# Kernel tuning notes

Hardware: AMD Instinct MI355X
Metric: run time of the kernel (lower is better)

## Reference

```python
import jax, jax.numpy as jnp
import numpy as np

HIDDEN = 1024
NUM_HEADS = 16
HEAD_DIM = HIDDEN // NUM_HEADS
EPS = 1e-12


def _layernorm(x, g, b):
    mu = jnp.mean(x, axis=-1, keepdims=True)
    var = jnp.var(x, axis=-1, keepdims=True)
    return (x - mu) * jax.lax.rsqrt(var + EPS) * g + b


def _attention(q, k, v, mask, Wd, bd, ln_g, ln_b):
    # q: [B,T,H], k/v: [B,S,H], mask: [B,1,1,S] additive
    B, T, _ = q.shape
    S = k.shape[1]
    qh = q.reshape(B, T, NUM_HEADS, HEAD_DIM).transpose(0, 2, 1, 3)  # [B,h,T,d]
    kh = k.reshape(B, S, NUM_HEADS, HEAD_DIM).transpose(0, 2, 1, 3)
    vh = v.reshape(B, S, NUM_HEADS, HEAD_DIM).transpose(0, 2, 1, 3)
    scores = jnp.einsum('bhtd,bhsd->bhts', qh, kh) / jnp.sqrt(jnp.float32(HEAD_DIM))
    if mask is not None:
        scores = scores + mask
    probs = jax.nn.softmax(scores, axis=-1)  # dropout = identity in eval
    ctx = jnp.einsum('bhts,bhsd->bthd', probs, vh)  # [B,T,h,d]
    # torch: w = dense.weight.t().view(h, d, H); einsum('bfnd,ndh->bfh')
    w = Wd.T.reshape(NUM_HEADS, HEAD_DIM, HIDDEN)
    proj = jnp.einsum('bthd,hdH->btH', ctx, w) + bd
    # residual is the (projected) query tensor q, per source
    return _layernorm(q + proj, ln_g, ln_b)


def setup_inputs() -> dict:
    key = jax.random.key(0)
    ks = jax.random.split(key, 12)
    s = 0.02
    B, S, T = 4, 1024, 1024
    return {
        'encoder_states': jax.random.normal(ks[0], (B, S, HIDDEN), jnp.float32),
        'decoder_inputs': jax.random.normal(ks[1], (B, T, HIDDEN), jnp.float32),
        'src_attention_mask': jnp.zeros((B, 1, 1, S), jnp.float32),
        'tgt_attention_mask': jnp.zeros((B, 1, 1, T), jnp.float32),
        'Wq': jax.random.normal(ks[2], (HIDDEN, HIDDEN), jnp.float32) * s,
        'bq': jnp.zeros((HIDDEN,), jnp.float32),
        'Wk': jax.random.normal(ks[3], (HIDDEN, HIDDEN), jnp.float32) * s,
        'bk': jnp.zeros((HIDDEN,), jnp.float32),
        'Wv': jax.random.normal(ks[4], (HIDDEN, HIDDEN), jnp.float32) * s,
        'bv': jnp.zeros((HIDDEN,), jnp.float32),
        'Wd': jax.random.normal(ks[5], (HIDDEN, HIDDEN), jnp.float32) * s,
        'bd': jnp.zeros((HIDDEN,), jnp.float32),
        'ln_g': jnp.ones((HIDDEN,), jnp.float32),
        'ln_b': jnp.zeros((HIDDEN,), jnp.float32),
    }


def reference(encoder_states, decoder_inputs, src_attention_mask, tgt_attention_mask,
              Wq, bq, Wk, bk, Wv, bv, Wd, bd, ln_g, ln_b):
    # projections (torch Linear: x @ W.T + b)
    q1 = decoder_inputs @ Wq.T + bq
    k1 = decoder_inputs @ Wk.T + bk
    v1 = decoder_inputs @ Wv.T + bv
    ek = encoder_states @ Wk.T + bk
    ev = encoder_states @ Wv.T + bv
    # self-attention over decoder states
    self_out = _attention(q1, k1, v1, tgt_attention_mask, Wd, bd, ln_g, ln_b)
    # cross-attention: query = self_out directly (no extra projection, per source)
    out = _attention(self_out, ek, ev, src_attention_mask, Wd, bd, ln_g, ln_b)
    return out
```

## Files before the change

kernel.cpp:

```cpp
#include <hip/hip_runtime.h>
#include <stdint.h>


#define B_   4
#define T_   1024
#define S_   1024
#define H_   1024
#define LOG2E 1.44269504088896340736f
#define SCALE_K (0.125f * LOG2E)

typedef __attribute__((ext_vector_type(8)))  __bf16       bf16x8;
typedef __attribute__((ext_vector_type(4)))  float        f32x4;
typedef __attribute__((ext_vector_type(16))) float        f32x16;
typedef __attribute__((ext_vector_type(4)))  unsigned int uint4v;

static __device__ __forceinline__ float bf2f(unsigned int u) {
    return __builtin_bit_cast(float, u << 16);
}
static __device__ __forceinline__ unsigned short f2bf(float f) {
    unsigned int x = __builtin_bit_cast(unsigned int, f);
    return (unsigned short)((x + 0x7fffu + ((x >> 16) & 1u)) >> 16);
}
static __device__ __forceinline__ unsigned int cvt_pk_bf16(float lo, float hi) {
    unsigned int r;
    asm("v_cvt_pk_bf16_f32 %0, %1, %2" : "=v"(r) : "v"(lo), "v"(hi));
    return r;
}
static __device__ __forceinline__ void perm32swap(unsigned int& a, unsigned int& b) {
    asm("v_permlane32_swap_b32 %0, %1" : "+v"(a), "+v"(b));
}
static __device__ __forceinline__ f32x4 mfma16(bf16x8 a, bf16x8 b, f32x4 c) {
    return __builtin_amdgcn_mfma_f32_16x16x32_bf16(a, b, c, 0, 0, 0);
}
static __device__ __forceinline__ f32x16 mfma32(bf16x8 a, bf16x8 b, f32x16 c) {
    return __builtin_amdgcn_mfma_f32_32x32x16_bf16(a, b, c, 0, 0, 0);
}

typedef const __attribute__((address_space(1))) void gv_t;
typedef __attribute__((address_space(3))) void lv_t;
static __device__ __forceinline__ void g2lds16(const void* g, void* l) {
    __builtin_amdgcn_global_load_lds((gv_t*)(size_t)g, (lv_t*)(unsigned int)(size_t)l, 16, 0, 0);
}

struct CvtArgs {
    const float* src[6];
    unsigned short* dst[6];
    float scale[6];
    int n4[6];
};
__global__ __launch_bounds__(256)
void cvt_multi(CvtArgs a) {
    const int k = blockIdx.y;
    const int i = blockIdx.x * 256 + threadIdx.x;
    if (i >= a.n4[k]) return;
    const float s = a.scale[k];
    float4 v = ((const float4*)a.src[k])[i];
    uint2 o;
    o.x = (unsigned)f2bf(v.x * s) | ((unsigned)f2bf(v.y * s) << 16);
    o.y = (unsigned)f2bf(v.z * s) | ((unsigned)f2bf(v.w * s) << 16);
    ((uint2*)a.dst[k])[i] = o;
}

struct GemmJob {
    const unsigned short* A[5];
    const unsigned short* W[5];
    const float* bias[5];
    float bs[5];
    unsigned short* O[5];
    unsigned short* OT[5];
};
__global__ __launch_bounds__(256, 2)
void gemm_bf16(GemmJob job)
{
    __shared__ char smem[32768];
    char* As = smem;
    char* Bs = smem + 16384;
    const int tid = threadIdx.x;
    const int lane = tid & 63;
    const int w = tid >> 6;
    const int c = lane & 15, g = lane >> 4;
    const int wm = (w >> 1) * 64, wn = (w & 1) * 64;
    const int m0 = blockIdx.x * 128;
    const int set = blockIdx.y >> 3;
    const int n0 = (blockIdx.y & 7) * 128;
    const unsigned short* A    = job.A[set];
    const unsigned short* W    = job.W[set];
    const float* bias          = job.bias[set];
    const float bscale         = job.bs[set];
    unsigned short* O          = job.O[set];
    unsigned short* OT         = job.OT[set];

    f32x4 acc[4][4];
#pragma unroll
    for (int i = 0; i < 4; i++)
#pragma unroll
        for (int j = 0; j < 4; j++) acc[i][j] = (f32x4){0.f, 0.f, 0.f, 0.f};

    const int srow = w * 32 + (lane >> 3);
    const int swzc = ((lane & 7) ^ (lane >> 3)) * 8;
    const unsigned short* gA = A + (size_t)(m0 + srow) * 1024 + swzc;
    const unsigned short* gB = W + (size_t)(n0 + srow) * 1024 + swzc;
    char* lA = As + w * 4096;
    char* lB = Bs + w * 4096;

    for (int kk = 0; kk < 1024; kk += 64) {
#pragma unroll
        for (int q = 0; q < 4; q++) {
            g2lds16(gA + kk + q*8192, lA + q*1024);
            g2lds16(gB + kk + q*8192, lB + q*1024);
        }
        __syncthreads();
#pragma unroll
        for (int ksub = 0; ksub < 2; ksub++) {
            bf16x8 af[4], bfr[4];
#pragma unroll
            for (int t = 0; t < 4; t++) {
                const int ra = wm + t*16 + c;
                const int rb = wn + t*16 + c;
                const int so = ((ksub*4 + g) ^ (c & 7)) << 4;
                af[t]  = *(const bf16x8*)(As + ra*128 + so);
                bfr[t] = *(const bf16x8*)(Bs + rb*128 + so);
            }
#pragma unroll
            for (int i = 0; i < 4; i++)
#pragma unroll
                for (int j = 0; j < 4; j++)
                    acc[i][j] = mfma16(af[i], bfr[j], acc[i][j]);
        }
        __syncthreads();
    }

    float bvv[4];
#pragma unroll
    for (int j = 0; j < 4; j++) bvv[j] = bias[n0 + wn + j*16 + c] * bscale;
    char* eb = As + w * 4096;
#pragma unroll
    for (int p = 0; p < 2; p++) {
#pragma unroll
        for (int ii = 0; ii < 2; ii++) {
            const int i = p*2 + ii;
#pragma unroll
            for (int j = 0; j < 4; j++)
#pragma unroll
                for (int r = 0; r < 4; r++)
                    *(unsigned short*)(eb + (ii*16 + g*4 + r)*128 + (c + j*16)*2)
                        = f2bf(acc[i][j][r] + bvv[j]);
        }
        asm volatile("s_waitcnt lgkmcnt(0)" ::: "memory");
        if (OT == nullptr) {
#pragma unroll
            for (int it = 0; it < 4; it++) {
                const int lrow = it*8 + (lane >> 3);
                uint4 vv = *(const uint4*)(eb + lrow*128 + (lane & 7)*16);
                *(uint4*)(O + (size_t)(m0 + wm + p*32 + lrow)*1024 + n0 + wn + (lane & 7)*8) = vv;
            }
        } else {
            const int n_glob = n0 + wn + lane;
            const int hh = n_glob >> 6, dd = n_glob & 63;
            const int bidx = m0 >> 10;
            const int s_base = (m0 & 1023) + wm + p*32;
            unsigned short* vout = OT + ((size_t)((bidx*16 + hh)*64 + dd))*S_ + s_base;
            unsigned int pk[16];
#pragma unroll
            for (int r = 0; r < 16; r++) {
                unsigned int lo = *(const unsigned short*)(eb + (2*r    )*128 + lane*2);
                unsigned int hi = *(const unsigned short*)(eb + (2*r + 1)*128 + lane*2);
                pk[r] = lo | (hi << 16);
            }
#pragma unroll
            for (int q = 0; q < 4; q++) {
                uint4 vv;
                vv.x = pk[q*4 + 0]; vv.y = pk[q*4 + 1];
                vv.z = pk[q*4 + 2]; vv.w = pk[q*4 + 3];
                *(uint4*)(vout + q*8) = vv;
            }
        }
        if (p == 0) asm volatile("s_waitcnt lgkmcnt(0)" ::: "memory");
    }
}

__global__ __launch_bounds__(256, 4)
void attn_fused2(const unsigned short* __restrict__ Q,
                 const unsigned short* __restrict__ Kx,
                 const unsigned short* __restrict__ VT,
                 const float* __restrict__ mask,
                 unsigned short* __restrict__ Octx)
{
    __shared__ char smem[32768 + 4096 + 512 + 16];
    float* mb   = (float*)(smem + 32768);
    float* lbuf = (float*)(smem + 32768 + 4096);
    int* flag   = (int*)(smem + 32768 + 4096 + 512);

    const int tid = threadIdx.x;
    const int lane = tid & 63, w = tid >> 6;
    const int qc = lane & 31, hi = lane >> 5;
    const int bh = blockIdx.y, b = bh >> 4, h = bh & 15;
    const int q0 = blockIdx.x * 128 + w * 32;

    const int r0 = tid >> 3, sg = tid & 7;
    const unsigned short* gK0 = Kx + (size_t)(b*S_ + r0)*H_  + h*64 + sg*8;
    const unsigned short* gK1 = gK0 + (size_t)32*H_;
    const unsigned short* gV0 = VT + (size_t)(bh*64 + r0)*S_ + sg*8;
    const unsigned short* gV1 = gV0 + (size_t)32*S_;
    const int woff = r0*128 + ((sg*16) ^ ((r0 & 7) << 4));

    const unsigned short* qptr = Q + (size_t)(b*T_ + q0 + qc)*H_ + h*64 + hi*8;
    bf16x8 qf[4];
#pragma unroll
    for (int s = 0; s < 4; s++) qf[s] = *(const bf16x8*)(qptr + s*16);

    uint4 cK0 = *(const uint4*)gK0;
    uint4 cK1 = *(const uint4*)gK1;
    uint4 cV0 = *(const uint4*)gV0;
    uint4 cV1 = *(const uint4*)gV1;

    if (tid == 0) *flag = 0;
    __syncthreads();
    {
        float4 mv = ((const float4*)(mask + (size_t)b*S_))[tid];
        float4 ms;
        ms.x = mv.x * LOG2E; ms.y = mv.y * LOG2E; ms.z = mv.z * LOG2E; ms.w = mv.w * LOG2E;
        ((float4*)mb)[tid] = ms;
        if (mv.x != 0.f || mv.y != 0.f || mv.z != 0.f || mv.w != 0.f) atomicOr(flag, 1);
    }
    {
        char* b0 = smem;
        *(uint4*)(b0 + woff)               = cK0;
        *(uint4*)(b0 + 4096 + woff)        = cK1;
        *(uint4*)(b0 + 8192 + woff)        = cV0;
        *(uint4*)(b0 + 8192 + 4096 + woff) = cV1;
    }
    __syncthreads();
    const int msk = *flag;

    f32x16 o0 = {}, o1 = {};
    float lacc = 0.f;

    for (int t = 0; t < 16; ++t) {
        uint4 nK0, nK1, nV0, nV1;
        if (t < 15) {
            const size_t ko = (size_t)(t + 1) * 64 * H_;
            const int    vo = (t + 1) * 64;
            nK0 = *(const uint4*)(gK0 + ko);
            nK1 = *(const uint4*)(gK1 + ko);
            nV0 = *(const uint4*)(gV0 + vo);
            nV1 = *(const uint4*)(gV1 + vo);
        }
        char* Ks = smem + (t & 1) * 16384;
        char* Vs = Ks + 8192;

#pragma unroll
        for (int ts = 0; ts < 2; ++ts) {
            f32x16 st = {};
            __builtin_amdgcn_s_setprio(1);
#pragma unroll
            for (int step = 0; step < 4; ++step) {
                bf16x8 ak = *(const bf16x8*)(Ks + (ts*32 + qc)*128 +
                             ((step*32 + hi*16) ^ ((qc & 7) << 4)));
                st = mfma32(ak, qf[step], st);
            }
            __builtin_amdgcn_s_setprio(0);

            float pv[16];
            if (msk) {
#pragma unroll
                for (int rq = 0; rq < 4; ++rq) {
                    const float4 bb = *(const float4*)(mb + t*64 + ts*32 + rq*8 + hi*4);
#pragma unroll
                    for (int e = 0; e < 4; ++e)
                        pv[rq*4 + e] = __builtin_amdgcn_exp2f(st[rq*4 + e] + (&bb.x)[e]);
                }
            } else {
#pragma unroll
                for (int r = 0; r < 16; ++r) pv[r] = __builtin_amdgcn_exp2f(st[r]);
            }
#pragma unroll
            for (int r = 0; r < 16; ++r) lacc += pv[r];

#pragma unroll
            for (int half = 0; half < 2; ++half) {
                unsigned w0 = cvt_pk_bf16(pv[half*8 + 0], pv[half*8 + 1]);
                unsigned w1 = cvt_pk_bf16(pv[half*8 + 2], pv[half*8 + 3]);
                unsigned w2 = cvt_pk_bf16(pv[half*8 + 4], pv[half*8 + 5]);
                unsigned w3 = cvt_pk_bf16(pv[half*8 + 6], pv[half*8 + 7]);
                perm32swap(w0, w2);
                perm32swap(w1, w3);
                uint4v fw; fw[0] = w0; fw[1] = w1; fw[2] = w2; fw[3] = w3;
                const bf16x8 pa = __builtin_bit_cast(bf16x8, fw);
                const int scol = (ts*64 + half*32 + hi*16) ^ ((qc & 7) << 4);
                bf16x8 v0 = *(const bf16x8*)(Vs + qc*128        + scol);
                bf16x8 v1 = *(const bf16x8*)(Vs + (32 + qc)*128 + scol);
                __builtin_amdgcn_s_setprio(1);
                o0 = mfma32(pa, v0, o0);
                o1 = mfma32(pa, v1, o1);
                __builtin_amdgcn_s_setprio(0);
            }
        }

        if (t < 15) {
            char* nxt = smem + ((t + 1) & 1) * 16384;
            *(uint4*)(nxt + woff)               = nK0;
            *(uint4*)(nxt + 4096 + woff)        = nK1;
            *(uint4*)(nxt + 8192 + woff)        = nV0;
            *(uint4*)(nxt + 8192 + 4096 + woff) = nV1;
        }
        __syncthreads();
    }

    {
        unsigned la = __builtin_bit_cast(unsigned, lacc);
        unsigned lb = la;
        perm32swap(la, lb);
        const float ltot = __builtin_bit_cast(float, la) + __builtin_bit_cast(float, lb);
        const float linv = 1.f / ltot;
        if (hi == 0) lbuf[w*32 + qc] = linv;
    }
    __syncthreads();
    float4 li[4];
#pragma unroll
    for (int rq = 0; rq < 4; ++rq)
        li[rq] = *(const float4*)(lbuf + w*32 + rq*8 + hi*4);

#pragma unroll
    for (int dt = 0; dt < 2; ++dt) {
        const f32x16& oo = dt ? o1 : o0;
#pragma unroll
        for (int r = 0; r < 16; ++r) {
            const int qrow = (r & 3) + 8*(r >> 2) + 4*hi;
            const float val = oo[r] * (&li[r >> 2].x)[r & 3];
            Octx[(size_t)(b*T_ + q0 + qrow)*H_ + h*64 + dt*32 + qc] = f2bf(val);
        }
    }
}

template<int OUTMODE>
__global__ __launch_bounds__(256)
void ln_kernel(const unsigned short* __restrict__ resid,
               const unsigned short* __restrict__ proj,
               const float* __restrict__ gam,
               const float* __restrict__ bet,
               unsigned short* __restrict__ obf,
               float* __restrict__ of32)
{
    __shared__ float red[8];
    const int tid = threadIdx.x;
    const int lane = tid & 63, w = tid >> 6;
    const int i = tid * 4;
    const size_t base = (size_t)blockIdx.x * 1024 + i;
    uint2 rv = *(const uint2*)(resid + base);
    uint2 pv = *(const uint2*)(proj + base);
    float x[4];
    x[0] = bf2f(rv.x & 0xffffu) + bf2f(pv.x & 0xffffu);
    x[1] = bf2f(rv.x >> 16)     + bf2f(pv.x >> 16);
    x[2] = bf2f(rv.y & 0xffffu) + bf2f(pv.y & 0xffffu);
    x[3] = bf2f(rv.y >> 16)     + bf2f(pv.y >> 16);
    float s = x[0] + x[1] + x[2] + x[3];
    float q = x[0]*x[0] + x[1]*x[1] + x[2]*x[2] + x[3]*x[3];
#pragma unroll
    for (int off = 1; off < 64; off <<= 1) {
        s += __shfl_xor(s, off);
        q += __shfl_xor(q, off);
    }
    if (lane == 0) { red[w*2] = s; red[w*2 + 1] = q; }
    __syncthreads();
    s = red[0] + red[2] + red[4] + red[6];
    q = red[1] + red[3] + red[5] + red[7];
    const float mu   = s * (1.f/1024.f);
    const float var  = q * (1.f/1024.f) - mu*mu;
    const float rstd = rsqrtf(var + 1e-12f);
    const float4 gv = *(const float4*)(gam + i);
    const float4 bv = *(const float4*)(bet + i);
    float y[4];
#pragma unroll
    for (int j = 0; j < 4; j++)
        y[j] = (x[j] - mu) * rstd * (&gv.x)[j] + (&bv.x)[j];
    if (OUTMODE == 0) {
        uint2 oo;
        oo.x = (unsigned)f2bf(y[0]) | ((unsigned)f2bf(y[1]) << 16);
        oo.y = (unsigned)f2bf(y[2]) | ((unsigned)f2bf(y[3]) << 16);
        *(uint2*)(obf + base) = oo;
    } else {
        float4 oo; oo.x = y[0]; oo.y = y[1]; oo.z = y[2]; oo.w = y[3];
        *(float4*)(of32 + base) = oo;
    }
}

extern "C" void kernel_launch(void* const* d_in, const int* in_sizes, int n_in,
                              void* d_out, int out_size, void* d_ws, size_t ws_size,
                              hipStream_t stream)
{
    const float* enc   = (const float*)d_in[0];
    const float* dec   = (const float*)d_in[1];
    const float* smask = (const float*)d_in[2];
    const float* tmask = (const float*)d_in[3];
    const float* Wq = (const float*)d_in[4];
    const float* bq = (const float*)d_in[5];
    const float* Wk = (const float*)d_in[6];
    const float* bk = (const float*)d_in[7];
    const float* Wv = (const float*)d_in[8];
    const float* bv = (const float*)d_in[9];
    const float* Wd = (const float*)d_in[10];
    const float* bd = (const float*)d_in[11];
    const float* lng = (const float*)d_in[12];
    const float* lnb = (const float*)d_in[13];
    float* out = (float*)d_out;

    char* ws = (char*)d_ws;
    const size_t MB = 1024ull * 1024ull;
    unsigned short* dec_bf = (unsigned short*)(ws + 0*MB);
    unsigned short* enc_bf = (unsigned short*)(ws + 8*MB);
    unsigned short* Wq_bf  = (unsigned short*)(ws + 16*MB);
    unsigned short* Wk_bf  = (unsigned short*)(ws + 18*MB);
    unsigned short* Wv_bf  = (unsigned short*)(ws + 20*MB);
    unsigned short* Wd_bf  = (unsigned short*)(ws + 22*MB);
    unsigned short* q1  = (unsigned short*)(ws + 24*MB);
    unsigned short* k1  = (unsigned short*)(ws + 32*MB);
    unsigned short* vt1 = (unsigned short*)(ws + 40*MB);
    unsigned short* ek  = (unsigned short*)(ws + 48*MB);
    unsigned short* evt = (unsigned short*)(ws + 56*MB);
    unsigned short* ctx      = dec_bf;
    unsigned short* proj     = enc_bf;
    unsigned short* self_out = k1;

    CvtArgs ca;
    ca.src[0] = dec; ca.dst[0] = dec_bf; ca.scale[0] = 1.f;      ca.n4[0] = 1048576;
    ca.src[1] = enc; ca.dst[1] = enc_bf; ca.scale[1] = 1.f;      ca.n4[1] = 1048576;
    ca.src[2] = Wq;  ca.dst[2] = Wq_bf;  ca.scale[2] = 1.f;      ca.n4[2] = 262144;
    ca.src[3] = Wk;  ca.dst[3] = Wk_bf;  ca.scale[3] = SCALE_K;  ca.n4[3] = 262144;
    ca.src[4] = Wv;  ca.dst[4] = Wv_bf;  ca.scale[4] = 1.f;      ca.n4[4] = 262144;
    ca.src[5] = Wd;  ca.dst[5] = Wd_bf;  ca.scale[5] = 1.f;      ca.n4[5] = 262144;
    cvt_multi<<<dim3(4096, 6), 256, 0, stream>>>(ca);

    GemmJob j1;
    j1.A[0] = dec_bf; j1.W[0] = Wq_bf; j1.bias[0] = bq; j1.bs[0] = 1.f;     j1.O[0] = q1; j1.OT[0] = nullptr;
    j1.A[1] = dec_bf; j1.W[1] = Wk_bf; j1.bias[1] = bk; j1.bs[1] = SCALE_K; j1.O[1] = k1; j1.OT[1] = nullptr;
    j1.A[2] = dec_bf; j1.W[2] = Wv_bf; j1.bias[2] = bv; j1.bs[2] = 1.f;     j1.O[2] = nullptr; j1.OT[2] = vt1;
    j1.A[3] = enc_bf; j1.W[3] = Wk_bf; j1.bias[3] = bk; j1.bs[3] = SCALE_K; j1.O[3] = ek; j1.OT[3] = nullptr;
    j1.A[4] = enc_bf; j1.W[4] = Wv_bf; j1.bias[4] = bv; j1.bs[4] = 1.f;     j1.O[4] = nullptr; j1.OT[4] = evt;
    gemm_bf16<<<dim3(32, 40), 256, 0, stream>>>(j1);

    GemmJob jd;
    for (int i = 0; i < 5; i++) {
        jd.A[i] = ctx; jd.W[i] = Wd_bf; jd.bias[i] = bd; jd.bs[i] = 1.f;
        jd.O[i] = proj; jd.OT[i] = nullptr;
    }

    attn_fused2<<<dim3(8, 64), 256, 0, stream>>>(q1, k1, vt1, tmask, ctx);
    gemm_bf16<<<dim3(32, 8), 256, 0, stream>>>(jd);
    ln_kernel<0><<<4096, 256, 0, stream>>>(q1, proj, lng, lnb, self_out, nullptr);

    attn_fused2<<<dim3(8, 64), 256, 0, stream>>>(self_out, ek, evt, smask, ctx);
    gemm_bf16<<<dim3(32, 8), 256, 0, stream>>>(jd);
    ln_kernel<1><<<4096, 256, 0, stream>>>(self_out, proj, lng, lnb, nullptr, out);
}
```

Measured before the change: 168.6 us.

## Rework transposed V epilogue staging and swap attention grid axes

The GEMM epilogue for the transposed V output now stages results in a per-wave transposed LDS buffer with a padded 72-byte row stride. Each lane writes packed 8-byte words, then reads contiguous 16-byte chunks, replacing 32 scalar 2-byte LDS reads per lane. This is meant to cut LDS instruction count and bank conflicts. The attention launch also swaps grid axes so consecutive blocks cover different batch-heads rather than different query tiles of the same head, which changes the block scheduling order and L2 reuse of K/V.

```diff
diff --git a/kernel.cpp b/kernel.cpp
--- a/kernel.cpp
+++ b/kernel.cpp
@@ -133,49 +133,62 @@
     float bvv[4];
 #pragma unroll
     for (int j = 0; j < 4; j++) bvv[j] = bias[n0 + wn + j*16 + c] * bscale;
-    char* eb = As + w * 4096;
-#pragma unroll
-    for (int p = 0; p < 2; p++) {
-#pragma unroll
-        for (int ii = 0; ii < 2; ii++) {
-            const int i = p*2 + ii;
-#pragma unroll
-            for (int j = 0; j < 4; j++)
-#pragma unroll
-                for (int r = 0; r < 4; r++)
-                    *(unsigned short*)(eb + (ii*16 + g*4 + r)*128 + (c + j*16)*2)
-                        = f2bf(acc[i][j][r] + bvv[j]);
-        }
-        asm volatile("s_waitcnt lgkmcnt(0)" ::: "memory");
-        if (OT == nullptr) {
+
+    if (OT == nullptr) {
+        char* eb = As + w * 4096;
+#pragma unroll
+        for (int p = 0; p < 2; p++) {
+#pragma unroll
+            for (int ii = 0; ii < 2; ii++) {
+                const int i = p*2 + ii;
+#pragma unroll
+                for (int j = 0; j < 4; j++)
+#pragma unroll
+                    for (int r = 0; r < 4; r++)
+                        *(unsigned short*)(eb + (ii*16 + g*4 + r)*128 + (c + j*16)*2)
+                            = f2bf(acc[i][j][r] + bvv[j]);
+            }
+            asm volatile("s_waitcnt lgkmcnt(0)" ::: "memory");
 #pragma unroll
             for (int it = 0; it < 4; it++) {
                 const int lrow = it*8 + (lane >> 3);
                 uint4 vv = *(const uint4*)(eb + lrow*128 + (lane & 7)*16);
                 *(uint4*)(O + (size_t)(m0 + wm + p*32 + lrow)*1024 + n0 + wn + (lane & 7)*8) = vv;
             }
-        } else {
-            const int n_glob = n0 + wn + lane;
-            const int hh = n_glob >> 6, dd = n_glob & 63;
-            const int bidx = m0 >> 10;
-            const int s_base = (m0 & 1023) + wm + p*32;
-            unsigned short* vout = OT + ((size_t)((bidx*16 + hh)*64 + dd))*S_ + s_base;
-            unsigned int pk[16];
-#pragma unroll
-            for (int r = 0; r < 16; r++) {
-                unsigned int lo = *(const unsigned short*)(eb + (2*r    )*128 + lane*2);
-                unsigned int hi = *(const unsigned short*)(eb + (2*r + 1)*128 + lane*2);
-                pk[r] = lo | (hi << 16);
-            }
+            if (p == 0) asm volatile("s_waitcnt lgkmcnt(0)" ::: "memory");
+        }
+    } else {
+        char* ebT = smem + w * 8192;
+        const int n_glob = n0 + wn + lane;
+        const int hh = n_glob >> 6, dd = n_glob & 63;
+        const int bidx = m0 >> 10;
+        unsigned short* vout0 = OT + ((size_t)((bidx*16 + hh)*64 + dd))*S_ + (m0 & 1023) + wm;
+#pragma unroll
+        for (int p = 0; p < 2; p++) {
+#pragma unroll
+            for (int ii = 0; ii < 2; ii++) {
+                const int i = p*2 + ii;
+#pragma unroll
+                for (int j = 0; j < 4; j++) {
+                    uint2 pw;
+                    pw.x = (unsigned)f2bf(acc[i][j][0] + bvv[j]) |
+                           ((unsigned)f2bf(acc[i][j][1] + bvv[j]) << 16);
+                    pw.y = (unsigned)f2bf(acc[i][j][2] + bvv[j]) |
+                           ((unsigned)f2bf(acc[i][j][3] + bvv[j]) << 16);
+                    *(uint2*)(ebT + (j*16 + c)*72 + (ii*16 + g*4)*2) = pw;
+                }
+            }
+            asm volatile("s_waitcnt lgkmcnt(0)" ::: "memory");
+            unsigned short* vout = vout0 + p*32;
 #pragma unroll
             for (int q = 0; q < 4; q++) {
-                uint4 vv;
-                vv.x = pk[q*4 + 0]; vv.y = pk[q*4 + 1];
-                vv.z = pk[q*4 + 2]; vv.w = pk[q*4 + 3];
+                uint2 r0 = *(const uint2*)(ebT + lane*72 + (q*2    )*8);
+                uint2 r1 = *(const uint2*)(ebT + lane*72 + (q*2 + 1)*8);
+                uint4 vv; vv.x = r0.x; vv.y = r0.y; vv.z = r1.x; vv.w = r1.y;
                 *(uint4*)(vout + q*8) = vv;
             }
-        }
-        if (p == 0) asm volatile("s_waitcnt lgkmcnt(0)" ::: "memory");
+            if (p == 0) asm volatile("s_waitcnt lgkmcnt(0)" ::: "memory");
+        }
     }
 }
 
@@ -194,8 +207,8 @@
     const int tid = threadIdx.x;
     const int lane = tid & 63, w = tid >> 6;
     const int qc = lane & 31, hi = lane >> 5;
-    const int bh = blockIdx.y, b = bh >> 4, h = bh & 15;
-    const int q0 = blockIdx.x * 128 + w * 32;
+    const int bh = blockIdx.x, b = bh >> 4, h = bh & 15;
+    const int q0 = blockIdx.y * 128 + w * 32;
 
     const int r0 = tid >> 3, sg = tid & 7;
     const unsigned short* gK0 = Kx + (size_t)(b*S_ + r0)*H_  + h*64 + sg*8;
@@ -445,11 +458,11 @@
         jd.O[i] = proj; jd.OT[i] = nullptr;
     }
 
-    attn_fused2<<<dim3(8, 64), 256, 0, stream>>>(q1, k1, vt1, tmask, ctx);
+    attn_fused2<<<dim3(64, 8), 256, 0, stream>>>(q1, k1, vt1, tmask, ctx);
     gemm_bf16<<<dim3(32, 8), 256, 0, stream>>>(jd);
     ln_kernel<0><<<4096, 256, 0, stream>>>(q1, proj, lng, lnb, self_out, nullptr);
 
-    attn_fused2<<<dim3(8, 64), 256, 0, stream>>>(self_out, ek, evt, smask, ctx);
+    attn_fused2<<<dim3(64, 8), 256, 0, stream>>>(self_out, ek, evt, smask, ctx);
     gemm_bf16<<<dim3(32, 8), 256, 0, stream>>>(jd);
     ln_kernel<1><<<4096, 256, 0, stream>>>(self_out, proj, lng, lnb, nullptr, out);
 }
```

New measurement: 165.9 us. No clear change (-1.6%).
